# Optimization experiments

Measured on AMD Instinct MI355X. Metric: run time of the kernel, lower is better.

## Reference

```python
import jax, jax.numpy as jnp
import numpy as np


def setup_inputs() -> dict:
    key = jax.random.key(0)
    k1, k2 = jax.random.split(key)
    B, S, D = 32, 2048, 1024
    decoder_hidden = jax.random.normal(k1, (1, B, D), dtype=jnp.float32)
    encoder_outputs = jax.random.normal(k2, (S, B, D), dtype=jnp.float32)
    return {"decoder_hidden": decoder_hidden, "encoder_outputs": encoder_outputs}


def reference(decoder_hidden, encoder_outputs):
    # decoder_hidden: (1, B, D); encoder_outputs: (S, B, D)
    query = decoder_hidden[0]                      # (B, D)
    kv = jnp.transpose(encoder_outputs, (1, 0, 2)) # (B, S, D)
    energy = jnp.einsum('bsd,bd->bs', kv, query)   # dot-product scores (B, S)
    attn_scores = jax.nn.softmax(energy, axis=-1)  # (B, S)
    attn_values = jnp.einsum('bsd,bs->bd', kv, attn_scores)  # (B, D)
    return (attn_values, attn_scores)
```

## Files before the change

kernel.cpp:

```cpp
#include <hip/hip_runtime.h>
#include <math.h>

#define BB 32
#define SS 2048
#define DD 1024
#define NCH 32
#define CHS 64


__global__ __launch_bounds__(256) void fused_pass(const float* __restrict__ q,
                                                  const float* __restrict__ enc,
                                                  float* __restrict__ energy,
                                                  float* __restrict__ partial,
                                                  float* __restrict__ ml) {
    int bc   = blockIdx.x;
    int b    = bc >> 5;
    int c    = bc & (NCH - 1);
    int tid  = threadIdx.x;
    int wid  = tid >> 6;
    int lane = tid & 63;
    __shared__ float red[2][4];

    float4 qv = ((const float4*)(q + (size_t)b * DD))[tid];

    int s0 = c * CHS;
    const float4* base = (const float4*)enc;
    const size_t rowstride = (size_t)BB * DD / 4;
    size_t idx = (size_t)(s0 * BB + b) * (DD / 4) + tid;

    float m = -1e30f, l = 0.f;
    float4 acc = {0.f, 0.f, 0.f, 0.f};
    float4 v = base[idx];

    for (int i = 0; i < CHS; ++i) {
        float4 vn = {0.f, 0.f, 0.f, 0.f};
        if (i + 1 < CHS) vn = base[idx + (size_t)(i + 1) * rowstride];

        float pd = v.x * qv.x + v.y * qv.y + v.z * qv.z + v.w * qv.w;
#pragma unroll
        for (int off = 32; off > 0; off >>= 1)
            pd += __shfl_xor(pd, off, 64);
        if (lane == 0) red[i & 1][wid] = pd;
        __syncthreads();
        float e = red[i & 1][0] + red[i & 1][1] + red[i & 1][2] + red[i & 1][3];

        if (tid == 0) energy[b * SS + s0 + i] = e;

        float mn    = fmaxf(m, e);
        float scale = __expf(m - mn);
        float p     = __expf(e - mn);
        l = l * scale + p;
        acc.x = acc.x * scale + p * v.x;
        acc.y = acc.y * scale + p * v.y;
        acc.z = acc.z * scale + p * v.z;
        acc.w = acc.w * scale + p * v.w;
        m = mn;
        v = vn;
    }

    ((float4*)(partial + (size_t)bc * DD))[tid] = acc;
    if (tid == 0) { ml[bc * 2] = m; ml[bc * 2 + 1] = l; }
}

__global__ __launch_bounds__(256) void merge_kernel(const float* __restrict__ partial,
                                                    const float* __restrict__ ml,
                                                    float* __restrict__ values,
                                                    float* __restrict__ ML) {
    int b   = blockIdx.x;
    int tid = threadIdx.x;
    __shared__ float sw[NCH];
    __shared__ float Lsh, Msh;

    if (tid == 0) {
        float M = -1e30f;
        for (int c2 = 0; c2 < NCH; ++c2) M = fmaxf(M, ml[(b * NCH + c2) * 2]);
        float L = 0.f;
        for (int c2 = 0; c2 < NCH; ++c2) {
            float w = __expf(ml[(b * NCH + c2) * 2] - M);
            sw[c2] = w;
            L += w * ml[(b * NCH + c2) * 2 + 1];
        }
        Msh = M; Lsh = L;
        ML[b * 2] = M; ML[b * 2 + 1] = L;
    }
    __syncthreads();

    float4 acc = {0.f, 0.f, 0.f, 0.f};
    for (int c2 = 0; c2 < NCH; ++c2) {
        float w = sw[c2];
        float4 p = ((const float4*)(partial + (size_t)(b * NCH + c2) * DD))[tid];
        acc.x += w * p.x; acc.y += w * p.y; acc.z += w * p.z; acc.w += w * p.w;
    }
    float inv = 1.f / Lsh;
    acc.x *= inv; acc.y *= inv; acc.z *= inv; acc.w *= inv;
    ((float4*)(values + (size_t)b * DD))[tid] = acc;
}

__global__ __launch_bounds__(256) void scores_kernel(const float* __restrict__ energy,
                                                     const float* __restrict__ ML,
                                                     float* __restrict__ scores) {
    int idx = blockIdx.x * 256 + threadIdx.x;
    int b   = idx >> 11;
    float M = ML[b * 2], L = ML[b * 2 + 1];
    scores[idx] = __expf(energy[idx] - M) / L;
}

extern "C" void kernel_launch(void* const* d_in, const int* in_sizes, int n_in,
                              void* d_out, int out_size, void* d_ws, size_t ws_size,
                              hipStream_t stream) {
    const float* q   = (const float*)d_in[0];
    const float* enc = (const float*)d_in[1];
    float* out    = (float*)d_out;
    float* values = out;
    float* scores = out + BB * DD;

    float* energy  = (float*)d_ws;
    float* partial = energy + BB * SS;
    float* ml      = partial + (size_t)BB * NCH * DD;
    float* ML      = ml + BB * NCH * 2;

    fused_pass<<<BB * NCH, 256, 0, stream>>>(q, enc, energy, partial, ml);
    merge_kernel<<<BB, 256, 0, stream>>>(partial, ml, values, ML);
    scores_kernel<<<(BB * SS) / 256, 256, 0, stream>>>(energy, ML, scores);
}
```

Before: 53.85 us.

## Give each wavefront its own row chunk and fuse scores into merge

The main pass now has each 64-lane wavefront own 16 sequence rows across the full D dimension with four float4 loads per row. Each row's dot product is reduced within the wavefront by shuffles, which removes the per-row block-wide __syncthreads. The four per-wave online-softmax partials are combined in shared memory before being written out. The separate scores kernel is folded into the merge kernel, dropping one launch and the ML round-trip. In exchange each block uses 16KB of shared memory and more registers per thread (launch bound hint of 4 blocks), and the score pass is limited to 32 blocks.

```diff
diff --git a/kernel.cpp b/kernel.cpp
--- a/kernel.cpp
+++ b/kernel.cpp
@@ -5,67 +5,98 @@
 #define SS 2048
 #define DD 1024
 #define NCH 32
-#define CHS 64
+#define WR 16
 
 
-__global__ __launch_bounds__(256) void fused_pass(const float* __restrict__ q,
-                                                  const float* __restrict__ enc,
-                                                  float* __restrict__ energy,
-                                                  float* __restrict__ partial,
-                                                  float* __restrict__ ml) {
-    int bc   = blockIdx.x;
-    int b    = bc >> 5;
-    int c    = bc & (NCH - 1);
-    int tid  = threadIdx.x;
-    int wid  = tid >> 6;
-    int lane = tid & 63;
-    __shared__ float red[2][4];
+__global__ __launch_bounds__(256, 4) void fused_pass(const float* __restrict__ q,
+                                                     const float* __restrict__ enc,
+                                                     float* __restrict__ energy,
+                                                     float* __restrict__ partial,
+                                                     float* __restrict__ ml) {
+    int blk = blockIdx.x;
+    int b   = blk >> 5;
+    int cb  = blk & (NCH - 1);
+    int tid = threadIdx.x;
+    int wid = tid >> 6;
+    int ln  = tid & 63;
 
-    float4 qv = ((const float4*)(q + (size_t)b * DD))[tid];
+    __shared__ float sm[4], sl[4];
+    __shared__ float sacc[4][DD];
 
-    int s0 = c * CHS;
+    const float4* qp = (const float4*)(q + (size_t)b * DD);
+    float4 qv[4];
+#pragma unroll
+    for (int k = 0; k < 4; ++k) qv[k] = qp[ln + 64 * k];
+
+    int s0 = cb * 64 + wid * WR;
     const float4* base = (const float4*)enc;
     const size_t rowstride = (size_t)BB * DD / 4;
-    size_t idx = (size_t)(s0 * BB + b) * (DD / 4) + tid;
+    size_t idx0 = (size_t)(s0 * BB + b) * (DD / 4) + ln;
 
     float m = -1e30f, l = 0.f;
-    float4 acc = {0.f, 0.f, 0.f, 0.f};
-    float4 v = base[idx];
+    float4 acc[4] = {{0,0,0,0},{0,0,0,0},{0,0,0,0},{0,0,0,0}};
 
-    for (int i = 0; i < CHS; ++i) {
-        float4 vn = {0.f, 0.f, 0.f, 0.f};
-        if (i + 1 < CHS) vn = base[idx + (size_t)(i + 1) * rowstride];
+#pragma unroll
+    for (int i = 0; i < WR; ++i) {
+        float4 v[4];
+#pragma unroll
+        for (int k = 0; k < 4; ++k)
+            v[k] = base[idx0 + (size_t)i * rowstride + k * 64];
 
-        float pd = v.x * qv.x + v.y * qv.y + v.z * qv.z + v.w * qv.w;
+        float pd = 0.f;
+#pragma unroll
+        for (int k = 0; k < 4; ++k)
+            pd += v[k].x * qv[k].x + v[k].y * qv[k].y
+                + v[k].z * qv[k].z + v[k].w * qv[k].w;
 #pragma unroll
         for (int off = 32; off > 0; off >>= 1)
             pd += __shfl_xor(pd, off, 64);
-        if (lane == 0) red[i & 1][wid] = pd;
-        __syncthreads();
-        float e = red[i & 1][0] + red[i & 1][1] + red[i & 1][2] + red[i & 1][3];
 
-        if (tid == 0) energy[b * SS + s0 + i] = e;
+        if (ln == 0) energy[b * SS + s0 + i] = pd;
 
-        float mn    = fmaxf(m, e);
+        float mn    = fmaxf(m, pd);
         float scale = __expf(m - mn);
-        float p     = __expf(e - mn);
+        float p     = __expf(pd - mn);
         l = l * scale + p;
-        acc.x = acc.x * scale + p * v.x;
-        acc.y = acc.y * scale + p * v.y;
-        acc.z = acc.z * scale + p * v.z;
-        acc.w = acc.w * scale + p * v.w;
+#pragma unroll
+        for (int k = 0; k < 4; ++k) {
+            acc[k].x = acc[k].x * scale + p * v[k].x;
+            acc[k].y = acc[k].y * scale + p * v[k].y;
+            acc[k].z = acc[k].z * scale + p * v[k].z;
+            acc[k].w = acc[k].w * scale + p * v[k].w;
+        }
         m = mn;
-        v = vn;
     }
 
-    ((float4*)(partial + (size_t)bc * DD))[tid] = acc;
-    if (tid == 0) { ml[bc * 2] = m; ml[bc * 2 + 1] = l; }
+    if (ln == 0) { sm[wid] = m; sl[wid] = l; }
+#pragma unroll
+    for (int k = 0; k < 4; ++k)
+        ((float4*)sacc[wid])[ln + 64 * k] = acc[k];
+    __syncthreads();
+
+    float M = fmaxf(fmaxf(sm[0], sm[1]), fmaxf(sm[2], sm[3]));
+    float w0 = __expf(sm[0] - M), w1 = __expf(sm[1] - M);
+    float w2 = __expf(sm[2] - M), w3 = __expf(sm[3] - M);
+    float L = w0 * sl[0] + w1 * sl[1] + w2 * sl[2] + w3 * sl[3];
+
+    float4 p0 = ((const float4*)sacc[0])[tid];
+    float4 p1 = ((const float4*)sacc[1])[tid];
+    float4 p2 = ((const float4*)sacc[2])[tid];
+    float4 p3 = ((const float4*)sacc[3])[tid];
+    float4 o;
+    o.x = w0 * p0.x + w1 * p1.x + w2 * p2.x + w3 * p3.x;
+    o.y = w0 * p0.y + w1 * p1.y + w2 * p2.y + w3 * p3.y;
+    o.z = w0 * p0.z + w1 * p1.z + w2 * p2.z + w3 * p3.z;
+    o.w = w0 * p0.w + w1 * p1.w + w2 * p2.w + w3 * p3.w;
+    ((float4*)partial)[(size_t)blk * (DD / 4) + tid] = o;
+    if (tid == 0) { ml[blk * 2] = M; ml[blk * 2 + 1] = L; }
 }
 
-__global__ __launch_bounds__(256) void merge_kernel(const float* __restrict__ partial,
+__global__ __launch_bounds__(256) void merge_scores(const float* __restrict__ partial,
                                                     const float* __restrict__ ml,
+                                                    const float* __restrict__ energy,
                                                     float* __restrict__ values,
-                                                    float* __restrict__ ML) {
+                                                    float* __restrict__ scores) {
     int b   = blockIdx.x;
     int tid = threadIdx.x;
     __shared__ float sw[NCH];
@@ -73,36 +104,32 @@
 
     if (tid == 0) {
         float M = -1e30f;
-        for (int c2 = 0; c2 < NCH; ++c2) M = fmaxf(M, ml[(b * NCH + c2) * 2]);
+        for (int c = 0; c < NCH; ++c) M = fmaxf(M, ml[(b * NCH + c) * 2]);
         float L = 0.f;
-        for (int c2 = 0; c2 < NCH; ++c2) {
-            float w = __expf(ml[(b * NCH + c2) * 2] - M);
-            sw[c2] = w;
-            L += w * ml[(b * NCH + c2) * 2 + 1];
+        for (int c = 0; c < NCH; ++c) {
+            float w = __expf(ml[(b * NCH + c) * 2] - M);
+            sw[c] = w;
+            L += w * ml[(b * NCH + c) * 2 + 1];
         }
         Msh = M; Lsh = L;
-        ML[b * 2] = M; ML[b * 2 + 1] = L;
     }
     __syncthreads();
+    float M = Msh, inv = 1.f / Lsh;
 
     float4 acc = {0.f, 0.f, 0.f, 0.f};
-    for (int c2 = 0; c2 < NCH; ++c2) {
-        float w = sw[c2];
-        float4 p = ((const float4*)(partial + (size_t)(b * NCH + c2) * DD))[tid];
+    for (int c = 0; c < NCH; ++c) {
+        float w = sw[c];
+        float4 p = ((const float4*)partial)[(size_t)(b * NCH + c) * (DD / 4) + tid];
         acc.x += w * p.x; acc.y += w * p.y; acc.z += w * p.z; acc.w += w * p.w;
     }
-    float inv = 1.f / Lsh;
     acc.x *= inv; acc.y *= inv; acc.z *= inv; acc.w *= inv;
-    ((float4*)(values + (size_t)b * DD))[tid] = acc;
-}
+    ((float4*)values)[(size_t)b * (DD / 4) + tid] = acc;
 
-__global__ __launch_bounds__(256) void scores_kernel(const float* __restrict__ energy,
-                                                     const float* __restrict__ ML,
-                                                     float* __restrict__ scores) {
-    int idx = blockIdx.x * 256 + threadIdx.x;
-    int b   = idx >> 11;
-    float M = ML[b * 2], L = ML[b * 2 + 1];
-    scores[idx] = __expf(energy[idx] - M) / L;
+#pragma unroll
+    for (int k = 0; k < 8; ++k) {
+        int idx = b * SS + k * 256 + tid;
+        scores[idx] = __expf(energy[idx] - M) * inv;
+    }
 }
 
 extern "C" void kernel_launch(void* const* d_in, const int* in_sizes, int n_in,
@@ -117,9 +144,7 @@
     float* energy  = (float*)d_ws;
     float* partial = energy + BB * SS;
     float* ml      = partial + (size_t)BB * NCH * DD;
-    float* ML      = ml + BB * NCH * 2;
 
     fused_pass<<<BB * NCH, 256, 0, stream>>>(q, enc, energy, partial, ml);
-    merge_kernel<<<BB, 256, 0, stream>>>(partial, ml, values, ML);
-    scores_kernel<<<(BB * SS) / 256, 256, 0, stream>>>(energy, ML, scores);
+    merge_scores<<<BB, 256, 0, stream>>>(partial, ml, energy, values, scores);
 }
```

After: 130.0 us. +141.3%, slower.

## Double split-K chunk count and fuse merge with score normalization

Applied to the files above, without the earlier changes.

The first pass can now split the sequence into 64 chunks per batch instead of 32, when the workspace is large enough, with an occupancy hint of 8 blocks per SM. This doubles the number of blocks so the memory-bound streaming pass has more in-flight loads. The separate merge and scores kernels are combined into one kernel that launches four blocks per batch row, each computing the global max and sum redundantly, which removes one launch. The cost is twice as much partial-accumulator traffic to write and read back in the merge step.

```diff
diff --git a/kernel.cpp b/kernel.cpp
--- a/kernel.cpp
+++ b/kernel.cpp
@@ -4,28 +4,29 @@
 #define BB 32
 #define SS 2048
 #define DD 1024
-#define NCH 32
-#define CHS 64
 
 
-__global__ __launch_bounds__(256) void fused_pass(const float* __restrict__ q,
-                                                  const float* __restrict__ enc,
-                                                  float* __restrict__ energy,
-                                                  float* __restrict__ partial,
-                                                  float* __restrict__ ml) {
-    int bc   = blockIdx.x;
-    int b    = bc >> 5;
-    int c    = bc & (NCH - 1);
-    int tid  = threadIdx.x;
-    int wid  = tid >> 6;
-    int lane = tid & 63;
+template <int NCH>
+__global__ __launch_bounds__(256, 8) void fused_pass(const float* __restrict__ q,
+                                                     const float* __restrict__ enc,
+                                                     float* __restrict__ energy,
+                                                     float* __restrict__ partial,
+                                                     float* __restrict__ ml) {
+    constexpr int CHS = SS / NCH;
+    int blk = blockIdx.x;
+    int b   = blk / NCH;
+    int cb  = blk % NCH;
+    int tid = threadIdx.x;
+    int wid = tid >> 6;
+    int ln  = tid & 63;
+
     __shared__ float red[2][4];
 
     float4 qv = ((const float4*)(q + (size_t)b * DD))[tid];
 
-    int s0 = c * CHS;
+    int s0 = cb * CHS;
     const float4* base = (const float4*)enc;
-    const size_t rowstride = (size_t)BB * DD / 4;
+    const size_t rs = (size_t)BB * (DD / 4);
     size_t idx = (size_t)(s0 * BB + b) * (DD / 4) + tid;
 
     float m = -1e30f, l = 0.f;
@@ -34,13 +35,13 @@
 
     for (int i = 0; i < CHS; ++i) {
         float4 vn = {0.f, 0.f, 0.f, 0.f};
-        if (i + 1 < CHS) vn = base[idx + (size_t)(i + 1) * rowstride];
+        if (i + 1 < CHS) vn = base[idx + (size_t)(i + 1) * rs];
 
         float pd = v.x * qv.x + v.y * qv.y + v.z * qv.z + v.w * qv.w;
 #pragma unroll
         for (int off = 32; off > 0; off >>= 1)
             pd += __shfl_xor(pd, off, 64);
-        if (lane == 0) red[i & 1][wid] = pd;
+        if (ln == 0) red[i & 1][wid] = pd;
         __syncthreads();
         float e = red[i & 1][0] + red[i & 1][1] + red[i & 1][2] + red[i & 1][3];
 
@@ -58,51 +59,46 @@
         v = vn;
     }
 
-    ((float4*)(partial + (size_t)bc * DD))[tid] = acc;
-    if (tid == 0) { ml[bc * 2] = m; ml[bc * 2 + 1] = l; }
+    ((float4*)(partial + (size_t)blk * DD))[tid] = acc;
+    if (tid == 0) { ml[blk * 2] = m; ml[blk * 2 + 1] = l; }
 }
 
-__global__ __launch_bounds__(256) void merge_kernel(const float* __restrict__ partial,
+__global__ __launch_bounds__(256) void merge_scores(const float* __restrict__ partial,
                                                     const float* __restrict__ ml,
+                                                    const float* __restrict__ energy,
                                                     float* __restrict__ values,
-                                                    float* __restrict__ ML) {
-    int b   = blockIdx.x;
-    int tid = threadIdx.x;
-    __shared__ float sw[NCH];
-    __shared__ float Lsh, Msh;
+                                                    float* __restrict__ scores,
+                                                    int nch) {
+    int blk  = blockIdx.x;
+    int b    = blk >> 2;
+    int quad = blk & 3;
+    int tid  = threadIdx.x;
+    __shared__ float sm[64], sl[64];
 
-    if (tid == 0) {
-        float M = -1e30f;
-        for (int c2 = 0; c2 < NCH; ++c2) M = fmaxf(M, ml[(b * NCH + c2) * 2]);
-        float L = 0.f;
-        for (int c2 = 0; c2 < NCH; ++c2) {
-            float w = __expf(ml[(b * NCH + c2) * 2] - M);
-            sw[c2] = w;
-            L += w * ml[(b * NCH + c2) * 2 + 1];
-        }
-        Msh = M; Lsh = L;
-        ML[b * 2] = M; ML[b * 2 + 1] = L;
+    if (tid < nch) {
+        sm[tid] = ml[(b * nch + tid) * 2];
+        sl[tid] = ml[(b * nch + tid) * 2 + 1];
     }
     __syncthreads();
 
-    float4 acc = {0.f, 0.f, 0.f, 0.f};
-    for (int c2 = 0; c2 < NCH; ++c2) {
-        float w = sw[c2];
-        float4 p = ((const float4*)(partial + (size_t)(b * NCH + c2) * DD))[tid];
-        acc.x += w * p.x; acc.y += w * p.y; acc.z += w * p.z; acc.w += w * p.w;
+    float M = -1e30f;
+    for (int c = 0; c < nch; ++c) M = fmaxf(M, sm[c]);
+
+    int d = quad * 256 + tid;
+    float L = 0.f, acc = 0.f;
+    for (int c = 0; c < nch; ++c) {
+        float w = __expf(sm[c] - M);
+        L += w * sl[c];
+        acc += w * partial[(size_t)(b * nch + c) * DD + d];
     }
-    float inv = 1.f / Lsh;
-    acc.x *= inv; acc.y *= inv; acc.z *= inv; acc.w *= inv;
-    ((float4*)(values + (size_t)b * DD))[tid] = acc;
-}
+    float inv = 1.f / L;
+    values[b * DD + d] = acc * inv;
 
-__global__ __launch_bounds__(256) void scores_kernel(const float* __restrict__ energy,
-                                                     const float* __restrict__ ML,
-                                                     float* __restrict__ scores) {
-    int idx = blockIdx.x * 256 + threadIdx.x;
-    int b   = idx >> 11;
-    float M = ML[b * 2], L = ML[b * 2 + 1];
-    scores[idx] = __expf(energy[idx] - M) / L;
+#pragma unroll
+    for (int k = 0; k < 2; ++k) {
+        int idx = b * SS + quad * 512 + k * 256 + tid;
+        scores[idx] = __expf(energy[idx] - M) * inv;
+    }
 }
 
 extern "C" void kernel_launch(void* const* d_in, const int* in_sizes, int n_in,
@@ -114,12 +110,17 @@
     float* values = out;
     float* scores = out + BB * DD;
 
+    size_t need64 = ((size_t)BB * SS + (size_t)BB * 64 * DD + (size_t)BB * 64 * 2)
+                    * sizeof(float);
+    int nch = (ws_size >= need64) ? 64 : 32;
+
     float* energy  = (float*)d_ws;
     float* partial = energy + BB * SS;
-    float* ml      = partial + (size_t)BB * NCH * DD;
-    float* ML      = ml + BB * NCH * 2;
+    float* ml      = partial + (size_t)BB * nch * DD;
 
-    fused_pass<<<BB * NCH, 256, 0, stream>>>(q, enc, energy, partial, ml);
-    merge_kernel<<<BB, 256, 0, stream>>>(partial, ml, values, ML);
-    scores_kernel<<<(BB * SS) / 256, 256, 0, stream>>>(energy, ML, scores);
+    if (nch == 64)
+        fused_pass<64><<<BB * 64, 256, 0, stream>>>(q, enc, energy, partial, ml);
+    else
+        fused_pass<32><<<BB * 32, 256, 0, stream>>>(q, enc, energy, partial, ml);
+    merge_scores<<<BB * 4, 256, 0, stream>>>(partial, ml, energy, values, scores, nch);
 }
```

Measured after the change: 55.00 us. 2.1% more time.
